# Performance work log

Hardware: AMD Instinct MI355X
Metric: run time of the kernel (lower is better)

Reference implementation:

```python
import jax, jax.numpy as jnp
import numpy as np

N_NODES = 10000
N_EDGES = 160000
MUL = 16          # multiplicity (num_radial channels) per irrep
EMB = 64          # radial_embed_size
HID = 128         # radial_hidden_size
N_PATHS = 5       # (0,0,0),(1,1,0),(0,1,1),(1,0,1),(1,1,1)
W_NUMEL = N_PATHS * MUL * MUL  # 1280


def setup_inputs() -> dict:
    key = jax.random.key(0)
    ks = jax.random.split(key, 9)
    return {
        'edge_index': jax.random.randint(ks[0], (2, N_EDGES), 0, N_NODES),
        'node_feat': jax.random.normal(ks[1], (N_NODES, 4 * MUL), dtype=jnp.float32),
        'edge_feat': jax.random.normal(ks[2], (N_EDGES, 4), dtype=jnp.float32),
        'edge_embed': jax.random.normal(ks[3], (N_EDGES, EMB), dtype=jnp.float32),
        'fc_w1': jax.random.normal(ks[4], (EMB, HID), dtype=jnp.float32),
        'fc_w2': jax.random.normal(ks[5], (HID, HID), dtype=jnp.float32),
        'fc_w3': jax.random.normal(ks[6], (HID, W_NUMEL), dtype=jnp.float32),
        'sc_w0': jax.random.normal(ks[7], (MUL, MUL), dtype=jnp.float32),
        'sc_w1': jax.random.normal(ks[8], (MUL, MUL), dtype=jnp.float32),
    }


def reference(edge_index, node_feat, edge_feat, edge_embed,
              fc_w1, fc_w2, fc_w3, sc_w0, sc_w1):
    """InfGCN GCNLayer: gather src features, fully-connected e3nn-style tensor
    product (irreps '16x0e+16x1o' x SH '1x0e+1x1o' -> '16x0e+16x1o') with
    per-edge weights from a radial MLP, scatter-add into dst, plus o3.Linear
    self-connection. e3nn conventions: FullyConnectedNet normalizes each layer
    by 1/sqrt(fan_in), component irrep_normalization gives w3j factors 1/sqrt(3)
    (1x1->0 dot) and 1/sqrt(2) (1x1->1 cross), element path_normalization gives
    per-path 1/sqrt(mul_in)."""
    E = edge_embed.shape[0]
    N = node_feat.shape[0]
    src, dst = edge_index[0], edge_index[1]

    # radial network (silu on hidden layers, e3nn fan-in normalization)
    h = jax.nn.silu(edge_embed @ (fc_w1 / np.sqrt(EMB)))
    h = jax.nn.silu(h @ (fc_w2 / np.sqrt(HID)))
    w = (h @ (fc_w3 / np.sqrt(HID))).reshape(E, N_PATHS, MUL, MUL)  # [E,P,u,w]

    # gather + split src features into l=0 / l=1 parts
    x = node_feat[src]                       # [E, 64]
    x0 = x[:, :MUL]                          # [E, u]
    x1 = x[:, MUL:].reshape(E, MUL, 3)       # [E, u, 3]
    y0 = edge_feat[:, :1]                    # [E, 1]
    y1 = edge_feat[:, 1:4]                   # [E, 3]

    inv = 1.0 / np.sqrt(MUL)                 # path fan-in normalization
    # l=0 output: paths (0,0,0) and (1,1,0)
    dot = jnp.einsum('eud,ed->eu', x1, y1) / np.sqrt(3.0)
    o0 = (jnp.einsum('euw,eu->ew', w[:, 0], x0 * y0)
          + jnp.einsum('euw,eu->ew', w[:, 1], dot)) * inv     # [E, w]
    # l=1 output: paths (0,1,1), (1,0,1), (1,1,1)
    cross = jnp.cross(x1, y1[:, None, :]) / np.sqrt(2.0)       # [E, u, 3]
    o1 = (jnp.einsum('euw,eu,ed->ewd', w[:, 2], x0, y1)
          + jnp.einsum('euw,eud->ewd', w[:, 3], x1 * y0[:, :, None])
          + jnp.einsum('euw,eud->ewd', w[:, 4], cross)) * inv  # [E, w, 3]

    msg = jnp.concatenate([o0, o1.reshape(E, 3 * MUL)], axis=-1)  # [E, 64]
    out = jax.ops.segment_sum(msg, dst, num_segments=N)            # [N, 64]

    # self-connection: o3.Linear, per-l channel mixing
    s0 = (node_feat[:, :MUL] @ sc_w0) * inv
    s1 = jnp.einsum('nud,uw->nwd', node_feat[:, MUL:].reshape(N, MUL, 3), sc_w1) * inv
    return out + jnp.concatenate([s0, s1.reshape(N, 3 * MUL)], axis=-1)
```

## Files before the change

### kernel.cpp

```cpp
#include <hip/hip_runtime.h>

#define NNODES 10000
#define NEDGES 160000
#define MUL 16
#define EMB 64
#define HID 128

#define RS128 0.08838834764831845f
#define SC3   (0.08838834764831845f * 0.25f)

typedef __attribute__((ext_vector_type(8))) _Float16 half8;
typedef __attribute__((ext_vector_type(4))) _Float16 half4;
typedef __attribute__((ext_vector_type(4))) float f32x4;

__global__ __launch_bounds__(256) void selfconn_kernel(
    const float* __restrict__ node_feat,
    const float* __restrict__ sc_w0,
    const float* __restrict__ sc_w1,
    float* __restrict__ out)
{
    const int tid = threadIdx.x;
    const int nl = tid >> 4;
    const int wp = tid & 15;
    const int n  = blockIdx.x * 16 + nl;

    __shared__ float nf[16][64];
    __shared__ float w0s[16][16];
    __shared__ float w1s[16][16];

    ((float4*)nf)[tid] = ((const float4*)(node_feat + (size_t)blockIdx.x * 16 * 64))[tid];
    if (tid < 64)       ((float4*)w0s)[tid]      = ((const float4*)sc_w0)[tid];
    else if (tid < 128) ((float4*)w1s)[tid - 64] = ((const float4*)sc_w1)[tid - 64];
    __syncthreads();

    float o0 = 0.f, o1x = 0.f, o1y = 0.f, o1z = 0.f;
#pragma unroll
    for (int u = 0; u < 16; ++u) {
        o0 += nf[nl][u] * w0s[u][wp];
        const float wv = w1s[u][wp];
        o1x += nf[nl][16 + u * 3 + 0] * wv;
        o1y += nf[nl][16 + u * 3 + 1] * wv;
        o1z += nf[nl][16 + u * 3 + 2] * wv;
    }
    float* op = out + (size_t)n * 64;
    op[wp]              = o0  * 0.25f;
    op[16 + wp * 3 + 0] = o1x * 0.25f;
    op[16 + wp * 3 + 1] = o1y * 0.25f;
    op[16 + wp * 3 + 2] = o1z * 0.25f;
}

__global__ __launch_bounds__(256) void prep_kernel(
    const float* __restrict__ w1,
    const float* __restrict__ w2,
    const float* __restrict__ w3,
    _Float16* __restrict__ wp)
{
    int idx = blockIdx.x * 256 + threadIdx.x;
    if (idx < 8192) {
        int j = idx & 7, lane = (idx >> 3) & 63, ks = (idx >> 9) & 1, nt = idx >> 10;
        int k = ks * 32 + (lane >> 4) * 8 + j;
        int n = nt * 16 + (lane & 15);
        wp[idx] = (_Float16)(w1[k * HID + n] * 0.125f);
    } else if (idx < 24576) {
        int t = idx - 8192;
        int j = t & 7, lane = (t >> 3) & 63, ks = (t >> 9) & 3, nt = t >> 11;
        int k = ks * 32 + (lane >> 4) * 8 + j;
        int n = nt * 16 + (lane & 15);
        wp[idx] = (_Float16)(w2[k * HID + n] * RS128);
    } else if (idx < 188416) {
        int t = idx - 24576;
        int j = t & 7, lane = (t >> 3) & 63, ks = (t >> 9) & 3, nt = t >> 11;
        int k = ks * 32 + (lane >> 4) * 8 + j;
        int n = nt * 16 + (lane & 15);
        wp[idx] = (_Float16)(w3[k * 1280 + n] * SC3);
    }
}

#define EE_OFF   0
#define H_OFF    4096
#define SA_OFF   12800
#define SB_OFF   15104
#define SXY_OFF  17408
#define SP3_OFF  23808
#define SP4_OFF  30208
#define SEF_OFF  36608
#define SIDX_OFF 37120
#define SMEM_BYTES 37376
#define OPW 65

__global__ __launch_bounds__(256, 4) void edge_mfma_kernel(
    const int*   __restrict__ ei,
    const float* __restrict__ node_feat,
    const float* __restrict__ edge_feat,
    const float* __restrict__ edge_embed,
    const _Float16* __restrict__ wpk,
    float* __restrict__ out)
{
    __shared__ __align__(16) char smem[SMEM_BYTES];

    const int tid = threadIdx.x;
    const int e0  = blockIdx.x * 32;

    int*   sidxp = (int*)(smem + SIDX_OFF);
    float* sEFp  = (float*)(smem + SEF_OFF);

    if (tid < 32)       sidxp[tid] = ei[e0 + tid];
    else if (tid < 64)  sidxp[tid] = ei[NEDGES + e0 + (tid - 32)];
    else if (tid < 192) {
        int t = tid - 64;
        sEFp[t] = edge_feat[e0 * 4 + t];
    }
    __syncthreads();

    float* xg = (float*)(smem + H_OFF);
    {
        const float4* eesrc = (const float4*)(edge_embed + (size_t)e0 * EMB);
#pragma unroll
        for (int it = 0; it < 2; ++it) {
            int f = tid + it * 256;
            int row = f >> 4, c4 = f & 15;
            float4 v = eesrc[f];
            half4 h = { (_Float16)v.x, (_Float16)v.y, (_Float16)v.z, (_Float16)v.w };
            *(half4*)(smem + EE_OFF + row * 128 + ((c4 * 8) ^ ((row & 7) << 4))) = h;

            int src = sidxp[row];
            float4 nv = ((const float4*)(node_feat + (size_t)src * 64))[c4];
            ((float4*)(xg + row * 68))[c4] = nv;
        }
    }
    __syncthreads();

#pragma unroll
    for (int it = 0; it < 2; ++it) {
        int el = (tid >> 4) + it * 16;
        int u  = tid & 15;
        const float* xr = xg + el * 68;
        float x0u = xr[u];
        float xa  = xr[16 + u * 3 + 0];
        float xb  = xr[16 + u * 3 + 1];
        float xc  = xr[16 + u * 3 + 2];
        float y0  = sEFp[el * 4 + 0];
        float y1x = sEFp[el * 4 + 1];
        float y1y = sEFp[el * 4 + 2];
        float y1z = sEFp[el * 4 + 3];
        *(float*)(smem + SA_OFF + u * 144 + el * 4) = x0u * y0;
        *(float*)(smem + SB_OFF + u * 144 + el * 4) =
            (xa * y1x + xb * y1y + xc * y1z) * 0.5773502691896258f;
        float* xy = (float*)(smem + SXY_OFF + u * 400 + el * 12);
        xy[0] = x0u * y1x; xy[1] = x0u * y1y; xy[2] = x0u * y1z;
        float* p3 = (float*)(smem + SP3_OFF + u * 400 + el * 12);
        p3[0] = xa * y0; p3[1] = xb * y0; p3[2] = xc * y0;
        float* p4 = (float*)(smem + SP4_OFF + u * 400 + el * 12);
        p4[0] = (xb * y1z - xc * y1y) * 0.7071067811865476f;
        p4[1] = (xc * y1x - xa * y1z) * 0.7071067811865476f;
        p4[2] = (xa * y1y - xb * y1x) * 0.7071067811865476f;
    }
    __syncthreads();

    const int lane  = tid & 63;
    const int w     = tid >> 6;
    const int wm    = w & 1;
    const int wn    = w >> 1;
    const int aswz  = (lane & 7) << 4;
    const int ako2  = (lane >> 4) * 16;
    const int ccol  = lane & 15;
    const int crow00 = (lane >> 4) * 4;

    const half8* w1p8 = (const half8*)wpk;
    const half8* w2p8 = (const half8*)(wpk + 8192);
    const half8* w3p8 = (const half8*)(wpk + 24576);

    {
        const int arow = wm * 16 + (lane & 15);
        half8 a0 = *(const half8*)(smem + EE_OFF + arow * 128 + ((ako2     ) ^ aswz));
        half8 a1 = *(const half8*)(smem + EE_OFF + arow * 128 + ((64 + ako2) ^ aswz));
        const int crow0 = wm * 16 + crow00;
#pragma unroll
        for (int i = 0; i < 4; ++i) {
            int nt = wn * 4 + i;
            f32x4 c = {0.f, 0.f, 0.f, 0.f};
            c = __builtin_amdgcn_mfma_f32_16x16x32_f16(a0, w1p8[(nt * 2 + 0) * 64 + lane], c, 0, 0, 0);
            c = __builtin_amdgcn_mfma_f32_16x16x32_f16(a1, w1p8[(nt * 2 + 1) * 64 + lane], c, 0, 0, 0);
#pragma unroll
            for (int r = 0; r < 4; ++r) {
                int row = crow0 + r;
                int col = nt * 16 + ccol;
                float x = c[r];
                float s = x / (1.f + __expf(-x));
                *(_Float16*)(smem + H_OFF + row * 256 + ((col * 2) ^ ((row & 7) << 4))) = (_Float16)s;
            }
        }
    }
    __syncthreads();

    {
        const int arow = wm * 16 + (lane & 15);
        half8 a2[4];
#pragma unroll
        for (int ks = 0; ks < 4; ++ks)
            a2[ks] = *(const half8*)(smem + H_OFF + arow * 256 + ((ks * 64 + ako2) ^ aswz));
        const int crow0 = wm * 16 + crow00;
        f32x4 cs[4];
#pragma unroll
        for (int i = 0; i < 4; ++i) {
            int nt = wn * 4 + i;
            f32x4 c = {0.f, 0.f, 0.f, 0.f};
#pragma unroll
            for (int ks = 0; ks < 4; ++ks)
                c = __builtin_amdgcn_mfma_f32_16x16x32_f16(a2[ks], w2p8[(nt * 4 + ks) * 64 + lane], c, 0, 0, 0);
            cs[i] = c;
        }
        __syncthreads();
#pragma unroll
        for (int i = 0; i < 4; ++i) {
            int nt = wn * 4 + i;
#pragma unroll
            for (int r = 0; r < 4; ++r) {
                int row = crow0 + r;
                int col = nt * 16 + ccol;
                float x = cs[i][r];
                float s = x / (1.f + __expf(-x));
                *(_Float16*)(smem + H_OFF + row * 256 + ((col * 2) ^ ((row & 7) << 4))) = (_Float16)s;
            }
        }
    }
    __syncthreads();

    half8 a3[2][4];
#pragma unroll
    for (int m = 0; m < 2; ++m) {
        const int arow = m * 16 + (lane & 15);
#pragma unroll
        for (int ks = 0; ks < 4; ++ks)
            a3[m][ks] = *(const half8*)(smem + H_OFF + arow * 256 + ((ks * 64 + ako2) ^ aswz));
    }

    float acc0[2][4] = {{0,0,0,0},{0,0,0,0}};
    float acc1[2][4][3] = {};

#define MM8(NT, C0, C1) { \
    const half8* bp = w3p8 + (size_t)(NT) * 256 + lane; \
    half8 b0 = bp[0], b1 = bp[64], b2 = bp[128], b3 = bp[192]; \
    C0 = __builtin_amdgcn_mfma_f32_16x16x32_f16(a3[0][0], b0, C0, 0, 0, 0); \
    C1 = __builtin_amdgcn_mfma_f32_16x16x32_f16(a3[1][0], b0, C1, 0, 0, 0); \
    C0 = __builtin_amdgcn_mfma_f32_16x16x32_f16(a3[0][1], b1, C0, 0, 0, 0); \
    C1 = __builtin_amdgcn_mfma_f32_16x16x32_f16(a3[1][1], b1, C1, 0, 0, 0); \
    C0 = __builtin_amdgcn_mfma_f32_16x16x32_f16(a3[0][2], b2, C0, 0, 0, 0); \
    C1 = __builtin_amdgcn_mfma_f32_16x16x32_f16(a3[1][2], b2, C1, 0, 0, 0); \
    C0 = __builtin_amdgcn_mfma_f32_16x16x32_f16(a3[0][3], b3, C0, 0, 0, 0); \
    C1 = __builtin_amdgcn_mfma_f32_16x16x32_f16(a3[1][3], b3, C1, 0, 0, 0); }

#define EPI_T(U, TOFF) { \
    const char* tb = smem + (TOFF) + (U) * 144 + crow00 * 4; \
    float4 t0 = *(const float4*)(tb); \
    float4 t1 = *(const float4*)(tb + 64); \
    acc0[0][0] += c0[0] * t0.x; acc0[0][1] += c0[1] * t0.y; \
    acc0[0][2] += c0[2] * t0.z; acc0[0][3] += c0[3] * t0.w; \
    acc0[1][0] += c1[0] * t1.x; acc0[1][1] += c1[1] * t1.y; \
    acc0[1][2] += c1[2] * t1.z; acc0[1][3] += c1[3] * t1.w; }

#define EPI_V(U, TOFF) { \
    const char* tb = smem + (TOFF) + (U) * 400 + crow00 * 12; \
    float4 q0 = *(const float4*)(tb);      \
    float4 q1 = *(const float4*)(tb + 16); \
    float4 q2 = *(const float4*)(tb + 32); \
    acc1[0][0][0] += c0[0]*q0.x; acc1[0][0][1] += c0[0]*q0.y; acc1[0][0][2] += c0[0]*q0.z; \
    acc1[0][1][0] += c0[1]*q0.w; acc1[0][1][1] += c0[1]*q1.x; acc1[0][1][2] += c0[1]*q1.y; \
    acc1[0][2][0] += c0[2]*q1.z; acc1[0][2][1] += c0[2]*q1.w; acc1[0][2][2] += c0[2]*q2.x; \
    acc1[0][3][0] += c0[3]*q2.y; acc1[0][3][1] += c0[3]*q2.z; acc1[0][3][2] += c0[3]*q2.w; \
    float4 p0 = *(const float4*)(tb + 192); \
    float4 p1 = *(const float4*)(tb + 208); \
    float4 p2 = *(const float4*)(tb + 224); \
    acc1[1][0][0] += c1[0]*p0.x; acc1[1][0][1] += c1[0]*p0.y; acc1[1][0][2] += c1[0]*p0.z; \
    acc1[1][1][0] += c1[1]*p0.w; acc1[1][1][1] += c1[1]*p1.x; acc1[1][1][2] += c1[1]*p1.y; \
    acc1[1][2][0] += c1[2]*p1.z; acc1[1][2][1] += c1[2]*p1.w; acc1[1][2][2] += c1[2]*p2.x; \
    acc1[1][3][0] += c1[3]*p2.y; acc1[1][3][1] += c1[3]*p2.z; acc1[1][3][2] += c1[3]*p2.w; }

#define TILE_T(NT, U, TOFF) { \
    f32x4 c0 = {0.f,0.f,0.f,0.f}, c1 = {0.f,0.f,0.f,0.f}; \
    MM8(NT, c0, c1); EPI_T(U, TOFF); }

#define TILE_V(NT, U, TOFF) { \
    f32x4 c0 = {0.f,0.f,0.f,0.f}, c1 = {0.f,0.f,0.f,0.f}; \
    MM8(NT, c0, c1); EPI_V(U, TOFF); }

    switch (w) {
    case 0:
#pragma unroll 4
        for (int u = 0; u < 16; ++u) TILE_T(u, u, SA_OFF);
#pragma unroll
        for (int u = 0; u < 4; ++u)  TILE_T(16 + u, u, SB_OFF);
        break;
    case 1:
#pragma unroll 4
        for (int u = 4; u < 16; ++u) TILE_T(16 + u, u, SB_OFF);
#pragma unroll 4
        for (int u = 0; u < 8; ++u)  TILE_V(32 + u, u, SXY_OFF);
        break;
    case 2:
#pragma unroll 4
        for (int u = 8; u < 16; ++u) TILE_V(32 + u, u, SXY_OFF);
#pragma unroll 4
        for (int u = 0; u < 12; ++u) TILE_V(48 + u, u, SP3_OFF);
        break;
    default:
#pragma unroll
        for (int u = 12; u < 16; ++u) TILE_V(48 + u, u, SP3_OFF);
#pragma unroll 4
        for (int u = 0; u < 16; ++u)  TILE_V(64 + u, u, SP4_OFF);
        break;
    }
#undef MM8
#undef EPI_T
#undef EPI_V
#undef TILE_T
#undef TILE_V

    __syncthreads();

    {
        float* myop = (float*)smem + w * 32 * OPW;
#pragma unroll
        for (int m = 0; m < 2; ++m)
#pragma unroll
            for (int r = 0; r < 4; ++r) {
                int row = crow00 + m * 16 + r;
                float* rp = myop + row * OPW;
                rp[ccol]              = acc0[m][r];
                rp[16 + ccol * 3 + 0] = acc1[m][r][0];
                rp[16 + ccol * 3 + 1] = acc1[m][r][1];
                rp[16 + ccol * 3 + 2] = acc1[m][r][2];
            }
    }
    __syncthreads();

    {
        const float* opf = (const float*)smem;
        const int rloc = lane >> 4;
#pragma unroll
        for (int rr = 0; rr < 2; ++rr) {
            int row = w * 8 + rr * 4 + rloc;
            int dst = sidxp[32 + row];
            float* op = out + (size_t)dst * 64;
            float v = opf[row * OPW + ccol]        + opf[2080 + row * OPW + ccol]
                    + opf[4160 + row * OPW + ccol] + opf[6240 + row * OPW + ccol];
            atomicAdd(op + ccol, v);
#pragma unroll
            for (int d = 0; d < 3; ++d) {
                int cc = 16 + ccol * 3 + d;
                float v1 = opf[row * OPW + cc]        + opf[2080 + row * OPW + cc]
                         + opf[4160 + row * OPW + cc] + opf[6240 + row * OPW + cc];
                atomicAdd(op + cc, v1);
            }
        }
    }
}

extern "C" void kernel_launch(void* const* d_in, const int* in_sizes, int n_in,
                              void* d_out, int out_size, void* d_ws, size_t ws_size,
                              hipStream_t stream) {
    const int*   ei         = (const int*)  d_in[0];
    const float* node_feat  = (const float*)d_in[1];
    const float* edge_feat  = (const float*)d_in[2];
    const float* edge_embed = (const float*)d_in[3];
    const float* fc_w1      = (const float*)d_in[4];
    const float* fc_w2      = (const float*)d_in[5];
    const float* fc_w3      = (const float*)d_in[6];
    const float* sc_w0      = (const float*)d_in[7];
    const float* sc_w1      = (const float*)d_in[8];
    float* out = (float*)d_out;
    _Float16* wpk = (_Float16*)d_ws;

    prep_kernel<<<736, 256, 0, stream>>>(fc_w1, fc_w2, fc_w3, wpk);
    selfconn_kernel<<<NNODES / 16, 256, 0, stream>>>(node_feat, sc_w0, sc_w1, out);
    edge_mfma_kernel<<<NEDGES / 32, 256, 0, stream>>>(ei, node_feat, edge_feat, edge_embed,
                                                      wpk, out);
}
```

Before: 150.4 us.

## Process 64 edges per block to halve weight B-fragment loads per edge

Doubles the edge tile per block from 32 to 64 edges, so each wave computes four 16-row M-subtiles against every loaded weight fragment. Previously the MLP layers split rows across waves and layer 3 used two subtiles. This cuts global/L2 traffic for the packed fp16 weights per edge, especially the large fc_w3 matrix. In exchange, LDS doubles to about 73 KB, launch bounds drop to 2 blocks per CU, and the larger accumulator arrays raise register pressure and may cost occupancy.

Result: slower. 175.1 us (+16.5%).

```diff
diff --git a/kernel.cpp b/kernel.cpp
--- a/kernel.cpp
+++ b/kernel.cpp
@@ -12,6 +12,8 @@
 typedef __attribute__((ext_vector_type(8))) _Float16 half8;
 typedef __attribute__((ext_vector_type(4))) _Float16 half4;
 typedef __attribute__((ext_vector_type(4))) float f32x4;
+
+#define MF(A, B, C) __builtin_amdgcn_mfma_f32_16x16x32_f16((A), (B), (C), 0, 0, 0)
 
 __global__ __launch_bounds__(256) void selfconn_kernel(
     const float* __restrict__ node_feat,
@@ -77,18 +79,18 @@
 }
 
 #define EE_OFF   0
-#define H_OFF    4096
-#define SA_OFF   12800
-#define SB_OFF   15104
-#define SXY_OFF  17408
-#define SP3_OFF  23808
-#define SP4_OFF  30208
-#define SEF_OFF  36608
-#define SIDX_OFF 37120
-#define SMEM_BYTES 37376
+#define H_OFF    8192
+#define SA_OFF   25600
+#define SB_OFF   29952
+#define SXY_OFF  34304
+#define SP3_OFF  46848
+#define SP4_OFF  59392
+#define SEF_OFF  71936
+#define SIDX_OFF 72960
+#define SMEM_BYTES 73472
 #define OPW 65
 
-__global__ __launch_bounds__(256, 4) void edge_mfma_kernel(
+__global__ __launch_bounds__(256, 2) void edge_mfma_kernel(
     const int*   __restrict__ ei,
     const float* __restrict__ node_feat,
     const float* __restrict__ edge_feat,
@@ -99,24 +101,21 @@
     __shared__ __align__(16) char smem[SMEM_BYTES];
 
     const int tid = threadIdx.x;
-    const int e0  = blockIdx.x * 32;
+    const int e0  = blockIdx.x * 64;
 
     int*   sidxp = (int*)(smem + SIDX_OFF);
     float* sEFp  = (float*)(smem + SEF_OFF);
 
-    if (tid < 32)       sidxp[tid] = ei[e0 + tid];
-    else if (tid < 64)  sidxp[tid] = ei[NEDGES + e0 + (tid - 32)];
-    else if (tid < 192) {
-        int t = tid - 64;
-        sEFp[t] = edge_feat[e0 * 4 + t];
-    }
+    if (tid < 64)       sidxp[tid] = ei[e0 + tid];
+    else if (tid < 128) sidxp[tid] = ei[NEDGES + e0 + (tid - 64)];
+    sEFp[tid] = edge_feat[e0 * 4 + tid];
     __syncthreads();
 
     float* xg = (float*)(smem + H_OFF);
     {
         const float4* eesrc = (const float4*)(edge_embed + (size_t)e0 * EMB);
 #pragma unroll
-        for (int it = 0; it < 2; ++it) {
+        for (int it = 0; it < 4; ++it) {
             int f = tid + it * 256;
             int row = f >> 4, c4 = f & 15;
             float4 v = eesrc[f];
@@ -131,7 +130,7 @@
     __syncthreads();
 
 #pragma unroll
-    for (int it = 0; it < 2; ++it) {
+    for (int it = 0; it < 4; ++it) {
         int el = (tid >> 4) + it * 16;
         int u  = tid & 15;
         const float* xr = xg + el * 68;
@@ -143,27 +142,25 @@
         float y1x = sEFp[el * 4 + 1];
         float y1y = sEFp[el * 4 + 2];
         float y1z = sEFp[el * 4 + 3];
-        *(float*)(smem + SA_OFF + u * 144 + el * 4) = x0u * y0;
-        *(float*)(smem + SB_OFF + u * 144 + el * 4) =
+        *(float*)(smem + SA_OFF + u * 272 + el * 4) = x0u * y0;
+        *(float*)(smem + SB_OFF + u * 272 + el * 4) =
             (xa * y1x + xb * y1y + xc * y1z) * 0.5773502691896258f;
-        float* xy = (float*)(smem + SXY_OFF + u * 400 + el * 12);
+        float* xy = (float*)(smem + SXY_OFF + u * 784 + el * 12);
         xy[0] = x0u * y1x; xy[1] = x0u * y1y; xy[2] = x0u * y1z;
-        float* p3 = (float*)(smem + SP3_OFF + u * 400 + el * 12);
+        float* p3 = (float*)(smem + SP3_OFF + u * 784 + el * 12);
         p3[0] = xa * y0; p3[1] = xb * y0; p3[2] = xc * y0;
-        float* p4 = (float*)(smem + SP4_OFF + u * 400 + el * 12);
+        float* p4 = (float*)(smem + SP4_OFF + u * 784 + el * 12);
         p4[0] = (xb * y1z - xc * y1y) * 0.7071067811865476f;
         p4[1] = (xc * y1x - xa * y1z) * 0.7071067811865476f;
         p4[2] = (xa * y1y - xb * y1x) * 0.7071067811865476f;
     }
     __syncthreads();
 
-    const int lane  = tid & 63;
-    const int w     = tid >> 6;
-    const int wm    = w & 1;
-    const int wn    = w >> 1;
-    const int aswz  = (lane & 7) << 4;
-    const int ako2  = (lane >> 4) * 16;
-    const int ccol  = lane & 15;
+    const int lane   = tid & 63;
+    const int w      = tid >> 6;
+    const int aswz   = (lane & 7) << 4;
+    const int ako2   = (lane >> 4) * 16;
+    const int ccol   = lane & 15;
     const int crow00 = (lane >> 4) * 4;
 
     const half8* w1p8 = (const half8*)wpk;
@@ -171,118 +168,132 @@
     const half8* w3p8 = (const half8*)(wpk + 24576);
 
     {
-        const int arow = wm * 16 + (lane & 15);
-        half8 a0 = *(const half8*)(smem + EE_OFF + arow * 128 + ((ako2     ) ^ aswz));
-        half8 a1 = *(const half8*)(smem + EE_OFF + arow * 128 + ((64 + ako2) ^ aswz));
-        const int crow0 = wm * 16 + crow00;
-#pragma unroll
-        for (int i = 0; i < 4; ++i) {
-            int nt = wn * 4 + i;
-            f32x4 c = {0.f, 0.f, 0.f, 0.f};
-            c = __builtin_amdgcn_mfma_f32_16x16x32_f16(a0, w1p8[(nt * 2 + 0) * 64 + lane], c, 0, 0, 0);
-            c = __builtin_amdgcn_mfma_f32_16x16x32_f16(a1, w1p8[(nt * 2 + 1) * 64 + lane], c, 0, 0, 0);
-#pragma unroll
-            for (int r = 0; r < 4; ++r) {
-                int row = crow0 + r;
-                int col = nt * 16 + ccol;
-                float x = c[r];
-                float s = x / (1.f + __expf(-x));
-                *(_Float16*)(smem + H_OFF + row * 256 + ((col * 2) ^ ((row & 7) << 4))) = (_Float16)s;
-            }
-        }
-    }
-    __syncthreads();
-
-    {
-        const int arow = wm * 16 + (lane & 15);
-        half8 a2[4];
+        half8 a1r[4][2];
+#pragma unroll
+        for (int ms = 0; ms < 4; ++ms) {
+            const int arow = ms * 16 + (lane & 15);
+            a1r[ms][0] = *(const half8*)(smem + EE_OFF + arow * 128 + ((ako2     ) ^ aswz));
+            a1r[ms][1] = *(const half8*)(smem + EE_OFF + arow * 128 + ((64 + ako2) ^ aswz));
+        }
+#pragma unroll
+        for (int i = 0; i < 2; ++i) {
+            const int nt = 2 * w + i;
+            const half8* b = w1p8 + (size_t)(nt * 2) * 64 + lane;
+            half8 b0 = b[0], b1 = b[64];
+            f32x4 c0 = {0,0,0,0}, c1 = {0,0,0,0}, c2 = {0,0,0,0}, c3 = {0,0,0,0};
+            c0 = MF(a1r[0][0], b0, c0); c1 = MF(a1r[1][0], b0, c1);
+            c2 = MF(a1r[2][0], b0, c2); c3 = MF(a1r[3][0], b0, c3);
+            c0 = MF(a1r[0][1], b1, c0); c1 = MF(a1r[1][1], b1, c1);
+            c2 = MF(a1r[2][1], b1, c2); c3 = MF(a1r[3][1], b1, c3);
+            f32x4 cs[4] = {c0, c1, c2, c3};
+#pragma unroll
+            for (int ms = 0; ms < 4; ++ms)
+#pragma unroll
+                for (int r = 0; r < 4; ++r) {
+                    int row = ms * 16 + crow00 + r;
+                    int col = nt * 16 + ccol;
+                    float x = cs[ms][r];
+                    float s = x / (1.f + __expf(-x));
+                    *(_Float16*)(smem + H_OFF + row * 256 + ((col * 2) ^ ((row & 7) << 4))) = (_Float16)s;
+                }
+        }
+    }
+    __syncthreads();
+
+    {
+        half8 a2r[4][4];
+#pragma unroll
+        for (int ms = 0; ms < 4; ++ms) {
+            const int arow = ms * 16 + (lane & 15);
+#pragma unroll
+            for (int ks = 0; ks < 4; ++ks)
+                a2r[ms][ks] = *(const half8*)(smem + H_OFF + arow * 256 + ((ks * 64 + ako2) ^ aswz));
+        }
+        f32x4 cs[2][4];
+#pragma unroll
+        for (int i = 0; i < 2; ++i) {
+            const int nt = 2 * w + i;
+            const half8* b = w2p8 + (size_t)(nt * 4) * 64 + lane;
+            half8 b0 = b[0], b1 = b[64], b2 = b[128], b3 = b[192];
+            f32x4 c0 = {0,0,0,0}, c1 = {0,0,0,0}, c2 = {0,0,0,0}, c3 = {0,0,0,0};
+            c0 = MF(a2r[0][0], b0, c0); c1 = MF(a2r[1][0], b0, c1);
+            c2 = MF(a2r[2][0], b0, c2); c3 = MF(a2r[3][0], b0, c3);
+            c0 = MF(a2r[0][1], b1, c0); c1 = MF(a2r[1][1], b1, c1);
+            c2 = MF(a2r[2][1], b1, c2); c3 = MF(a2r[3][1], b1, c3);
+            c0 = MF(a2r[0][2], b2, c0); c1 = MF(a2r[1][2], b2, c1);
+            c2 = MF(a2r[2][2], b2, c2); c3 = MF(a2r[3][2], b2, c3);
+            c0 = MF(a2r[0][3], b3, c0); c1 = MF(a2r[1][3], b3, c1);
+            c2 = MF(a2r[2][3], b3, c2); c3 = MF(a2r[3][3], b3, c3);
+            cs[i][0] = c0; cs[i][1] = c1; cs[i][2] = c2; cs[i][3] = c3;
+        }
+        __syncthreads();
+#pragma unroll
+        for (int i = 0; i < 2; ++i) {
+            const int nt = 2 * w + i;
+#pragma unroll
+            for (int ms = 0; ms < 4; ++ms)
+#pragma unroll
+                for (int r = 0; r < 4; ++r) {
+                    int row = ms * 16 + crow00 + r;
+                    int col = nt * 16 + ccol;
+                    float x = cs[i][ms][r];
+                    float s = x / (1.f + __expf(-x));
+                    *(_Float16*)(smem + H_OFF + row * 256 + ((col * 2) ^ ((row & 7) << 4))) = (_Float16)s;
+                }
+        }
+    }
+    __syncthreads();
+
+    half8 a3[4][4];
+#pragma unroll
+    for (int ms = 0; ms < 4; ++ms) {
+        const int arow = ms * 16 + (lane & 15);
 #pragma unroll
         for (int ks = 0; ks < 4; ++ks)
-            a2[ks] = *(const half8*)(smem + H_OFF + arow * 256 + ((ks * 64 + ako2) ^ aswz));
-        const int crow0 = wm * 16 + crow00;
-        f32x4 cs[4];
-#pragma unroll
-        for (int i = 0; i < 4; ++i) {
-            int nt = wn * 4 + i;
-            f32x4 c = {0.f, 0.f, 0.f, 0.f};
-#pragma unroll
-            for (int ks = 0; ks < 4; ++ks)
-                c = __builtin_amdgcn_mfma_f32_16x16x32_f16(a2[ks], w2p8[(nt * 4 + ks) * 64 + lane], c, 0, 0, 0);
-            cs[i] = c;
-        }
-        __syncthreads();
-#pragma unroll
-        for (int i = 0; i < 4; ++i) {
-            int nt = wn * 4 + i;
-#pragma unroll
-            for (int r = 0; r < 4; ++r) {
-                int row = crow0 + r;
-                int col = nt * 16 + ccol;
-                float x = cs[i][r];
-                float s = x / (1.f + __expf(-x));
-                *(_Float16*)(smem + H_OFF + row * 256 + ((col * 2) ^ ((row & 7) << 4))) = (_Float16)s;
-            }
-        }
-    }
-    __syncthreads();
-
-    half8 a3[2][4];
-#pragma unroll
-    for (int m = 0; m < 2; ++m) {
-        const int arow = m * 16 + (lane & 15);
-#pragma unroll
-        for (int ks = 0; ks < 4; ++ks)
-            a3[m][ks] = *(const half8*)(smem + H_OFF + arow * 256 + ((ks * 64 + ako2) ^ aswz));
-    }
-
-    float acc0[2][4] = {{0,0,0,0},{0,0,0,0}};
-    float acc1[2][4][3] = {};
-
-#define MM8(NT, C0, C1) { \
+            a3[ms][ks] = *(const half8*)(smem + H_OFF + arow * 256 + ((ks * 64 + ako2) ^ aswz));
+    }
+
+    float acc0[4][4] = {};
+    float acc1[4][4][3] = {};
+
+#define MM16(NT) \
     const half8* bp = w3p8 + (size_t)(NT) * 256 + lane; \
     half8 b0 = bp[0], b1 = bp[64], b2 = bp[128], b3 = bp[192]; \
-    C0 = __builtin_amdgcn_mfma_f32_16x16x32_f16(a3[0][0], b0, C0, 0, 0, 0); \
-    C1 = __builtin_amdgcn_mfma_f32_16x16x32_f16(a3[1][0], b0, C1, 0, 0, 0); \
-    C0 = __builtin_amdgcn_mfma_f32_16x16x32_f16(a3[0][1], b1, C0, 0, 0, 0); \
-    C1 = __builtin_amdgcn_mfma_f32_16x16x32_f16(a3[1][1], b1, C1, 0, 0, 0); \
-    C0 = __builtin_amdgcn_mfma_f32_16x16x32_f16(a3[0][2], b2, C0, 0, 0, 0); \
-    C1 = __builtin_amdgcn_mfma_f32_16x16x32_f16(a3[1][2], b2, C1, 0, 0, 0); \
-    C0 = __builtin_amdgcn_mfma_f32_16x16x32_f16(a3[0][3], b3, C0, 0, 0, 0); \
-    C1 = __builtin_amdgcn_mfma_f32_16x16x32_f16(a3[1][3], b3, C1, 0, 0, 0); }
-
-#define EPI_T(U, TOFF) { \
-    const char* tb = smem + (TOFF) + (U) * 144 + crow00 * 4; \
-    float4 t0 = *(const float4*)(tb); \
-    float4 t1 = *(const float4*)(tb + 64); \
-    acc0[0][0] += c0[0] * t0.x; acc0[0][1] += c0[1] * t0.y; \
-    acc0[0][2] += c0[2] * t0.z; acc0[0][3] += c0[3] * t0.w; \
-    acc0[1][0] += c1[0] * t1.x; acc0[1][1] += c1[1] * t1.y; \
-    acc0[1][2] += c1[2] * t1.z; acc0[1][3] += c1[3] * t1.w; }
-
-#define EPI_V(U, TOFF) { \
-    const char* tb = smem + (TOFF) + (U) * 400 + crow00 * 12; \
-    float4 q0 = *(const float4*)(tb);      \
-    float4 q1 = *(const float4*)(tb + 16); \
-    float4 q2 = *(const float4*)(tb + 32); \
-    acc1[0][0][0] += c0[0]*q0.x; acc1[0][0][1] += c0[0]*q0.y; acc1[0][0][2] += c0[0]*q0.z; \
-    acc1[0][1][0] += c0[1]*q0.w; acc1[0][1][1] += c0[1]*q1.x; acc1[0][1][2] += c0[1]*q1.y; \
-    acc1[0][2][0] += c0[2]*q1.z; acc1[0][2][1] += c0[2]*q1.w; acc1[0][2][2] += c0[2]*q2.x; \
-    acc1[0][3][0] += c0[3]*q2.y; acc1[0][3][1] += c0[3]*q2.z; acc1[0][3][2] += c0[3]*q2.w; \
-    float4 p0 = *(const float4*)(tb + 192); \
-    float4 p1 = *(const float4*)(tb + 208); \
-    float4 p2 = *(const float4*)(tb + 224); \
-    acc1[1][0][0] += c1[0]*p0.x; acc1[1][0][1] += c1[0]*p0.y; acc1[1][0][2] += c1[0]*p0.z; \
-    acc1[1][1][0] += c1[1]*p0.w; acc1[1][1][1] += c1[1]*p1.x; acc1[1][1][2] += c1[1]*p1.y; \
-    acc1[1][2][0] += c1[2]*p1.z; acc1[1][2][1] += c1[2]*p1.w; acc1[1][2][2] += c1[2]*p2.x; \
-    acc1[1][3][0] += c1[3]*p2.y; acc1[1][3][1] += c1[3]*p2.z; acc1[1][3][2] += c1[3]*p2.w; }
+    f32x4 c0 = {0,0,0,0}, c1 = {0,0,0,0}, c2 = {0,0,0,0}, c3 = {0,0,0,0}; \
+    c0 = MF(a3[0][0], b0, c0); c1 = MF(a3[1][0], b0, c1); \
+    c2 = MF(a3[2][0], b0, c2); c3 = MF(a3[3][0], b0, c3); \
+    c0 = MF(a3[0][1], b1, c0); c1 = MF(a3[1][1], b1, c1); \
+    c2 = MF(a3[2][1], b1, c2); c3 = MF(a3[3][1], b1, c3); \
+    c0 = MF(a3[0][2], b2, c0); c1 = MF(a3[1][2], b2, c1); \
+    c2 = MF(a3[2][2], b2, c2); c3 = MF(a3[3][2], b2, c3); \
+    c0 = MF(a3[0][3], b3, c0); c1 = MF(a3[1][3], b3, c1); \
+    c2 = MF(a3[2][3], b3, c2); c3 = MF(a3[3][3], b3, c3);
+
+#define EPIT1(CV, MS, TBB) { \
+    float4 t = *(const float4*)(TBB); \
+    acc0[MS][0] += CV[0] * t.x; acc0[MS][1] += CV[1] * t.y; \
+    acc0[MS][2] += CV[2] * t.z; acc0[MS][3] += CV[3] * t.w; }
+
+#define EPIV1(CV, MS, TBB) { \
+    float4 q0 = *(const float4*)(TBB); \
+    float4 q1 = *(const float4*)((TBB) + 16); \
+    float4 q2 = *(const float4*)((TBB) + 32); \
+    acc1[MS][0][0] += CV[0]*q0.x; acc1[MS][0][1] += CV[0]*q0.y; acc1[MS][0][2] += CV[0]*q0.z; \
+    acc1[MS][1][0] += CV[1]*q0.w; acc1[MS][1][1] += CV[1]*q1.x; acc1[MS][1][2] += CV[1]*q1.y; \
+    acc1[MS][2][0] += CV[2]*q1.z; acc1[MS][2][1] += CV[2]*q1.w; acc1[MS][2][2] += CV[2]*q2.x; \
+    acc1[MS][3][0] += CV[3]*q2.y; acc1[MS][3][1] += CV[3]*q2.z; acc1[MS][3][2] += CV[3]*q2.w; }
 
 #define TILE_T(NT, U, TOFF) { \
-    f32x4 c0 = {0.f,0.f,0.f,0.f}, c1 = {0.f,0.f,0.f,0.f}; \
-    MM8(NT, c0, c1); EPI_T(U, TOFF); }
+    MM16(NT); \
+    const char* tb = smem + (TOFF) + (U) * 272 + crow00 * 4; \
+    EPIT1(c0, 0, tb); EPIT1(c1, 1, tb + 64); \
+    EPIT1(c2, 2, tb + 128); EPIT1(c3, 3, tb + 192); }
 
 #define TILE_V(NT, U, TOFF) { \
-    f32x4 c0 = {0.f,0.f,0.f,0.f}, c1 = {0.f,0.f,0.f,0.f}; \
-    MM8(NT, c0, c1); EPI_V(U, TOFF); }
+    MM16(NT); \
+    const char* tb = smem + (TOFF) + (U) * 784 + crow00 * 12; \
+    EPIV1(c0, 0, tb); EPIV1(c1, 1, tb + 192); \
+    EPIV1(c2, 2, tb + 384); EPIV1(c3, 3, tb + 576); }
 
     switch (w) {
     case 0:
@@ -310,26 +321,26 @@
         for (int u = 0; u < 16; ++u)  TILE_V(64 + u, u, SP4_OFF);
         break;
     }
-#undef MM8
-#undef EPI_T
-#undef EPI_V
+#undef MM16
+#undef EPIT1
+#undef EPIV1
 #undef TILE_T
 #undef TILE_V
 
     __syncthreads();
 
     {
-        float* myop = (float*)smem + w * 32 * OPW;
-#pragma unroll
-        for (int m = 0; m < 2; ++m)
+        float* myop = (float*)smem + w * 64 * OPW;
+#pragma unroll
+        for (int ms = 0; ms < 4; ++ms)
 #pragma unroll
             for (int r = 0; r < 4; ++r) {
-                int row = crow00 + m * 16 + r;
+                int row = ms * 16 + crow00 + r;
                 float* rp = myop + row * OPW;
-                rp[ccol]              = acc0[m][r];
-                rp[16 + ccol * 3 + 0] = acc1[m][r][0];
-                rp[16 + ccol * 3 + 1] = acc1[m][r][1];
-                rp[16 + ccol * 3 + 2] = acc1[m][r][2];
+                rp[ccol]              = acc0[ms][r];
+                rp[16 + ccol * 3 + 0] = acc1[ms][r][0];
+                rp[16 + ccol * 3 + 1] = acc1[ms][r][1];
+                rp[16 + ccol * 3 + 2] = acc1[ms][r][2];
             }
     }
     __syncthreads();
@@ -338,18 +349,18 @@
         const float* opf = (const float*)smem;
         const int rloc = lane >> 4;
 #pragma unroll
-        for (int rr = 0; rr < 2; ++rr) {
-            int row = w * 8 + rr * 4 + rloc;
-            int dst = sidxp[32 + row];
+        for (int rr = 0; rr < 4; ++rr) {
+            int row = w * 16 + rr * 4 + rloc;
+            int dst = sidxp[64 + row];
             float* op = out + (size_t)dst * 64;
-            float v = opf[row * OPW + ccol]        + opf[2080 + row * OPW + ccol]
-                    + opf[4160 + row * OPW + ccol] + opf[6240 + row * OPW + ccol];
+            float v = opf[row * OPW + ccol]         + opf[4160 + row * OPW + ccol]
+                    + opf[8320 + row * OPW + ccol]  + opf[12480 + row * OPW + ccol];
             atomicAdd(op + ccol, v);
 #pragma unroll
             for (int d = 0; d < 3; ++d) {
                 int cc = 16 + ccol * 3 + d;
-                float v1 = opf[row * OPW + cc]        + opf[2080 + row * OPW + cc]
-                         + opf[4160 + row * OPW + cc] + opf[6240 + row * OPW + cc];
+                float v1 = opf[row * OPW + cc]         + opf[4160 + row * OPW + cc]
+                         + opf[8320 + row * OPW + cc]  + opf[12480 + row * OPW + cc];
                 atomicAdd(op + cc, v1);
             }
         }
@@ -373,6 +384,6 @@
 
     prep_kernel<<<736, 256, 0, stream>>>(fc_w1, fc_w2, fc_w3, wpk);
     selfconn_kernel<<<NNODES / 16, 256, 0, stream>>>(node_feat, sc_w0, sc_w1, out);
-    edge_mfma_kernel<<<NEDGES / 32, 256, 0, stream>>>(ei, node_feat, edge_feat, edge_embed,
+    edge_mfma_kernel<<<NEDGES / 64, 256, 0, stream>>>(ei, node_feat, edge_feat, edge_embed,
                                                       wpk, out);
 }
```

## Store edge tensor-product operands in fp16 and halve cross-wave reduction traffic

Applied to the files above, without the earlier changes.

The per-edge products (x0*y0, dot, x0*y1, x1*y0, cross) are now stored in shared memory as fp16 instead of fp32. This shrinks LDS use from about 37KB to 26KB per block and halves the epilogue LDS read bytes. The final reduction also changes: only waves 2-3 write partial sums to LDS, and waves 0-1 add those partials to their own registers before issuing the atomics. This costs precision on the epilogue operands and leaves half the waves idle during the atomic phase.

Result: slower. 226.5 us (+50.6%).

```diff
diff --git a/kernel.cpp b/kernel.cpp
--- a/kernel.cpp
+++ b/kernel.cpp
@@ -12,6 +12,8 @@
 typedef __attribute__((ext_vector_type(8))) _Float16 half8;
 typedef __attribute__((ext_vector_type(4))) _Float16 half4;
 typedef __attribute__((ext_vector_type(4))) float f32x4;
+
+#define MF(A, B, C) __builtin_amdgcn_mfma_f32_16x16x32_f16((A), (B), (C), 0, 0, 0)
 
 __global__ __launch_bounds__(256) void selfconn_kernel(
     const float* __restrict__ node_feat,
@@ -79,13 +81,13 @@
 #define EE_OFF   0
 #define H_OFF    4096
 #define SA_OFF   12800
-#define SB_OFF   15104
-#define SXY_OFF  17408
-#define SP3_OFF  23808
-#define SP4_OFF  30208
-#define SEF_OFF  36608
-#define SIDX_OFF 37120
-#define SMEM_BYTES 37376
+#define SB_OFF   14080
+#define SXY_OFF  15360
+#define SP3_OFF  18688
+#define SP4_OFF  22016
+#define SEF_OFF  25344
+#define SIDX_OFF 25856
+#define SMEM_BYTES 26112
 #define OPW 65
 
 __global__ __launch_bounds__(256, 4) void edge_mfma_kernel(
@@ -143,17 +145,21 @@
         float y1x = sEFp[el * 4 + 1];
         float y1y = sEFp[el * 4 + 2];
         float y1z = sEFp[el * 4 + 3];
-        *(float*)(smem + SA_OFF + u * 144 + el * 4) = x0u * y0;
-        *(float*)(smem + SB_OFF + u * 144 + el * 4) =
-            (xa * y1x + xb * y1y + xc * y1z) * 0.5773502691896258f;
-        float* xy = (float*)(smem + SXY_OFF + u * 400 + el * 12);
-        xy[0] = x0u * y1x; xy[1] = x0u * y1y; xy[2] = x0u * y1z;
-        float* p3 = (float*)(smem + SP3_OFF + u * 400 + el * 12);
-        p3[0] = xa * y0; p3[1] = xb * y0; p3[2] = xc * y0;
-        float* p4 = (float*)(smem + SP4_OFF + u * 400 + el * 12);
-        p4[0] = (xb * y1z - xc * y1y) * 0.7071067811865476f;
-        p4[1] = (xc * y1x - xa * y1z) * 0.7071067811865476f;
-        p4[2] = (xa * y1y - xb * y1x) * 0.7071067811865476f;
+        *(_Float16*)(smem + SA_OFF + u * 80 + el * 2) = (_Float16)(x0u * y0);
+        *(_Float16*)(smem + SB_OFF + u * 80 + el * 2) =
+            (_Float16)((xa * y1x + xb * y1y + xc * y1z) * 0.5773502691896258f);
+        _Float16* xy = (_Float16*)(smem + SXY_OFF + u * 208 + el * 6);
+        xy[0] = (_Float16)(x0u * y1x);
+        xy[1] = (_Float16)(x0u * y1y);
+        xy[2] = (_Float16)(x0u * y1z);
+        _Float16* p3 = (_Float16*)(smem + SP3_OFF + u * 208 + el * 6);
+        p3[0] = (_Float16)(xa * y0);
+        p3[1] = (_Float16)(xb * y0);
+        p3[2] = (_Float16)(xc * y0);
+        _Float16* p4 = (_Float16*)(smem + SP4_OFF + u * 208 + el * 6);
+        p4[0] = (_Float16)((xb * y1z - xc * y1y) * 0.7071067811865476f);
+        p4[1] = (_Float16)((xc * y1x - xa * y1z) * 0.7071067811865476f);
+        p4[2] = (_Float16)((xa * y1y - xb * y1x) * 0.7071067811865476f);
     }
     __syncthreads();
 
@@ -179,8 +185,8 @@
         for (int i = 0; i < 4; ++i) {
             int nt = wn * 4 + i;
             f32x4 c = {0.f, 0.f, 0.f, 0.f};
-            c = __builtin_amdgcn_mfma_f32_16x16x32_f16(a0, w1p8[(nt * 2 + 0) * 64 + lane], c, 0, 0, 0);
-            c = __builtin_amdgcn_mfma_f32_16x16x32_f16(a1, w1p8[(nt * 2 + 1) * 64 + lane], c, 0, 0, 0);
+            c = MF(a0, w1p8[(nt * 2 + 0) * 64 + lane], c);
+            c = MF(a1, w1p8[(nt * 2 + 1) * 64 + lane], c);
 #pragma unroll
             for (int r = 0; r < 4; ++r) {
                 int row = crow0 + r;
@@ -207,7 +213,7 @@
             f32x4 c = {0.f, 0.f, 0.f, 0.f};
 #pragma unroll
             for (int ks = 0; ks < 4; ++ks)
-                c = __builtin_amdgcn_mfma_f32_16x16x32_f16(a2[ks], w2p8[(nt * 4 + ks) * 64 + lane], c, 0, 0, 0);
+                c = MF(a2[ks], w2p8[(nt * 4 + ks) * 64 + lane], c);
             cs[i] = c;
         }
         __syncthreads();
@@ -241,40 +247,36 @@
 #define MM8(NT, C0, C1) { \
     const half8* bp = w3p8 + (size_t)(NT) * 256 + lane; \
     half8 b0 = bp[0], b1 = bp[64], b2 = bp[128], b3 = bp[192]; \
-    C0 = __builtin_amdgcn_mfma_f32_16x16x32_f16(a3[0][0], b0, C0, 0, 0, 0); \
-    C1 = __builtin_amdgcn_mfma_f32_16x16x32_f16(a3[1][0], b0, C1, 0, 0, 0); \
-    C0 = __builtin_amdgcn_mfma_f32_16x16x32_f16(a3[0][1], b1, C0, 0, 0, 0); \
-    C1 = __builtin_amdgcn_mfma_f32_16x16x32_f16(a3[1][1], b1, C1, 0, 0, 0); \
-    C0 = __builtin_amdgcn_mfma_f32_16x16x32_f16(a3[0][2], b2, C0, 0, 0, 0); \
-    C1 = __builtin_amdgcn_mfma_f32_16x16x32_f16(a3[1][2], b2, C1, 0, 0, 0); \
-    C0 = __builtin_amdgcn_mfma_f32_16x16x32_f16(a3[0][3], b3, C0, 0, 0, 0); \
-    C1 = __builtin_amdgcn_mfma_f32_16x16x32_f16(a3[1][3], b3, C1, 0, 0, 0); }
+    C0 = MF(a3[0][0], b0, C0); C1 = MF(a3[1][0], b0, C1); \
+    C0 = MF(a3[0][1], b1, C0); C1 = MF(a3[1][1], b1, C1); \
+    C0 = MF(a3[0][2], b2, C0); C1 = MF(a3[1][2], b2, C1); \
+    C0 = MF(a3[0][3], b3, C0); C1 = MF(a3[1][3], b3, C1); }
 
 #define EPI_T(U, TOFF) { \
-    const char* tb = smem + (TOFF) + (U) * 144 + crow00 * 4; \
-    float4 t0 = *(const float4*)(tb); \
-    float4 t1 = *(const float4*)(tb + 64); \
-    acc0[0][0] += c0[0] * t0.x; acc0[0][1] += c0[1] * t0.y; \
-    acc0[0][2] += c0[2] * t0.z; acc0[0][3] += c0[3] * t0.w; \
-    acc0[1][0] += c1[0] * t1.x; acc0[1][1] += c1[1] * t1.y; \
-    acc0[1][2] += c1[2] * t1.z; acc0[1][3] += c1[3] * t1.w; }
+    const char* tb = smem + (TOFF) + (U) * 80 + crow00 * 2; \
+    half4 t0 = *(const half4*)(tb); \
+    half4 t1 = *(const half4*)(tb + 32); \
+    acc0[0][0] += c0[0] * (float)t0[0]; acc0[0][1] += c0[1] * (float)t0[1]; \
+    acc0[0][2] += c0[2] * (float)t0[2]; acc0[0][3] += c0[3] * (float)t0[3]; \
+    acc0[1][0] += c1[0] * (float)t1[0]; acc0[1][1] += c1[1] * (float)t1[1]; \
+    acc0[1][2] += c1[2] * (float)t1[2]; acc0[1][3] += c1[3] * (float)t1[3]; }
 
 #define EPI_V(U, TOFF) { \
-    const char* tb = smem + (TOFF) + (U) * 400 + crow00 * 12; \
-    float4 q0 = *(const float4*)(tb);      \
-    float4 q1 = *(const float4*)(tb + 16); \
-    float4 q2 = *(const float4*)(tb + 32); \
-    acc1[0][0][0] += c0[0]*q0.x; acc1[0][0][1] += c0[0]*q0.y; acc1[0][0][2] += c0[0]*q0.z; \
-    acc1[0][1][0] += c0[1]*q0.w; acc1[0][1][1] += c0[1]*q1.x; acc1[0][1][2] += c0[1]*q1.y; \
-    acc1[0][2][0] += c0[2]*q1.z; acc1[0][2][1] += c0[2]*q1.w; acc1[0][2][2] += c0[2]*q2.x; \
-    acc1[0][3][0] += c0[3]*q2.y; acc1[0][3][1] += c0[3]*q2.z; acc1[0][3][2] += c0[3]*q2.w; \
-    float4 p0 = *(const float4*)(tb + 192); \
-    float4 p1 = *(const float4*)(tb + 208); \
-    float4 p2 = *(const float4*)(tb + 224); \
-    acc1[1][0][0] += c1[0]*p0.x; acc1[1][0][1] += c1[0]*p0.y; acc1[1][0][2] += c1[0]*p0.z; \
-    acc1[1][1][0] += c1[1]*p0.w; acc1[1][1][1] += c1[1]*p1.x; acc1[1][1][2] += c1[1]*p1.y; \
-    acc1[1][2][0] += c1[2]*p1.z; acc1[1][2][1] += c1[2]*p1.w; acc1[1][2][2] += c1[2]*p2.x; \
-    acc1[1][3][0] += c1[3]*p2.y; acc1[1][3][1] += c1[3]*p2.z; acc1[1][3][2] += c1[3]*p2.w; }
+    const char* tb = smem + (TOFF) + (U) * 208 + crow00 * 6; \
+    half4 q0 = *(const half4*)(tb); \
+    half4 q1 = *(const half4*)(tb + 8); \
+    half4 q2 = *(const half4*)(tb + 16); \
+    acc1[0][0][0] += c0[0]*(float)q0[0]; acc1[0][0][1] += c0[0]*(float)q0[1]; acc1[0][0][2] += c0[0]*(float)q0[2]; \
+    acc1[0][1][0] += c0[1]*(float)q0[3]; acc1[0][1][1] += c0[1]*(float)q1[0]; acc1[0][1][2] += c0[1]*(float)q1[1]; \
+    acc1[0][2][0] += c0[2]*(float)q1[2]; acc1[0][2][1] += c0[2]*(float)q1[3]; acc1[0][2][2] += c0[2]*(float)q2[0]; \
+    acc1[0][3][0] += c0[3]*(float)q2[1]; acc1[0][3][1] += c0[3]*(float)q2[2]; acc1[0][3][2] += c0[3]*(float)q2[3]; \
+    half4 p0 = *(const half4*)(tb + 96); \
+    half4 p1 = *(const half4*)(tb + 104); \
+    half4 p2 = *(const half4*)(tb + 112); \
+    acc1[1][0][0] += c1[0]*(float)p0[0]; acc1[1][0][1] += c1[0]*(float)p0[1]; acc1[1][0][2] += c1[0]*(float)p0[2]; \
+    acc1[1][1][0] += c1[1]*(float)p0[3]; acc1[1][1][1] += c1[1]*(float)p1[0]; acc1[1][1][2] += c1[1]*(float)p1[1]; \
+    acc1[1][2][0] += c1[2]*(float)p1[2]; acc1[1][2][1] += c1[2]*(float)p1[3]; acc1[1][2][2] += c1[2]*(float)p2[0]; \
+    acc1[1][3][0] += c1[3]*(float)p2[1]; acc1[1][3][1] += c1[3]*(float)p2[2]; acc1[1][3][2] += c1[3]*(float)p2[3]; }
 
 #define TILE_T(NT, U, TOFF) { \
     f32x4 c0 = {0.f,0.f,0.f,0.f}, c1 = {0.f,0.f,0.f,0.f}; \
@@ -318,8 +320,8 @@
 
     __syncthreads();
 
-    {
-        float* myop = (float*)smem + w * 32 * OPW;
+    if (w >= 2) {
+        float* myop = (float*)smem + (size_t)(w - 2) * 32 * OPW;
 #pragma unroll
         for (int m = 0; m < 2; ++m)
 #pragma unroll
@@ -334,25 +336,21 @@
     }
     __syncthreads();
 
-    {
-        const float* opf = (const float*)smem;
-        const int rloc = lane >> 4;
-#pragma unroll
-        for (int rr = 0; rr < 2; ++rr) {
-            int row = w * 8 + rr * 4 + rloc;
-            int dst = sidxp[32 + row];
-            float* op = out + (size_t)dst * 64;
-            float v = opf[row * OPW + ccol]        + opf[2080 + row * OPW + ccol]
-                    + opf[4160 + row * OPW + ccol] + opf[6240 + row * OPW + ccol];
-            atomicAdd(op + ccol, v);
-#pragma unroll
-            for (int d = 0; d < 3; ++d) {
-                int cc = 16 + ccol * 3 + d;
-                float v1 = opf[row * OPW + cc]        + opf[2080 + row * OPW + cc]
-                         + opf[4160 + row * OPW + cc] + opf[6240 + row * OPW + cc];
-                atomicAdd(op + cc, v1);
+    if (w < 2) {
+        const float* opf = (const float*)smem + (size_t)w * 32 * OPW;
+#pragma unroll
+        for (int m = 0; m < 2; ++m)
+#pragma unroll
+            for (int r = 0; r < 4; ++r) {
+                int row = crow00 + m * 16 + r;
+                const float* rp = opf + row * OPW;
+                int dst = sidxp[32 + row];
+                float* op = out + (size_t)dst * 64;
+                atomicAdd(op + ccol,              acc0[m][r]    + rp[ccol]);
+                atomicAdd(op + 16 + ccol * 3 + 0, acc1[m][r][0] + rp[16 + ccol * 3 + 0]);
+                atomicAdd(op + 16 + ccol * 3 + 1, acc1[m][r][1] + rp[16 + ccol * 3 + 1]);
+                atomicAdd(op + 16 + ccol * 3 + 2, acc1[m][r][2] + rp[16 + ccol * 3 + 2]);
             }
-        }
     }
 }
 
```
